# Kernel tuning notes

Measured on AMD Instinct MI355X. Metric: run time of the kernel, lower is better.

The kernel has to match this reference:

```python
import jax, jax.numpy as jnp
import numpy as np

N_NODES = 50000
N_EDGES = 400000
IN_CH = 5
HID = 64
HEADS = 8
NEG_SLOPE = 0.2  # PyG GATConv default


def _gat_layer(x, src, dst, n, W, a_src, a_dst, b, heads, C, concat):
    """PyG-style GATConv (eval mode, add_self_loops already applied to src/dst)."""
    h = (x @ W).reshape(n, heads, C)                      # [N,H,C]
    s_src = jnp.sum(h * a_src, axis=-1)                   # [N,H]
    s_dst = jnp.sum(h * a_dst, axis=-1)                   # [N,H]
    e = jax.nn.leaky_relu(s_src[src] + s_dst[dst], NEG_SLOPE)  # [E,H]
    # segment softmax over incoming edges of each dst node
    m = jax.ops.segment_max(e, dst, num_segments=n)       # [N,H]
    m = jnp.where(jnp.isfinite(m), m, 0.0)
    p = jnp.exp(e - m[dst])                               # [E,H]
    denom = jax.ops.segment_sum(p, dst, num_segments=n)   # [N,H]
    alpha = p / (denom[dst] + 1e-16)                      # [E,H]
    msg = alpha[:, :, None] * h[src]                      # [E,H,C]
    out = jax.ops.segment_sum(msg, dst, num_segments=n)   # [N,H,C]
    out = out.reshape(n, heads * C) if concat else out.mean(axis=1)
    return out + b


def setup_inputs() -> dict:
    key = jax.random.key(0)
    ks = jax.random.split(key, 16)
    g = lambda k, shape, fan: jax.random.normal(k, shape, jnp.float32) * (1.0 / np.sqrt(fan))
    x = jax.random.normal(ks[0], (N_NODES, IN_CH), jnp.float32)
    edge_index = jax.random.randint(ks[1], (2, N_EDGES), 0, N_NODES, dtype=jnp.int64)
    d = {
        "x": x,
        "edge_index": edge_index,
        # layer 1: in=5 -> 8 heads x 64
        "W1": g(ks[2], (IN_CH, HEADS * HID), IN_CH),
        "as1": g(ks[3], (HEADS, HID), HID),
        "ad1": g(ks[4], (HEADS, HID), HID),
        "b1": jnp.zeros((HEADS * HID,), jnp.float32),
        # layer 2: in=512 -> 8 heads x 64
        "W2": g(ks[5], (HEADS * HID, HEADS * HID), HEADS * HID),
        "as2": g(ks[6], (HEADS, HID), HID),
        "ad2": g(ks[7], (HEADS, HID), HID),
        "b2": jnp.zeros((HEADS * HID,), jnp.float32),
        # layer 3: in=512 -> 1 head x 64
        "W3": g(ks[8], (HEADS * HID, HID), HEADS * HID),
        "as3": g(ks[9], (1, HID), HID),
        "ad3": g(ks[10], (1, HID), HID),
        "b3": jnp.zeros((HID,), jnp.float32),
        # classifier
        "Wc": g(ks[11], (HID, 1), HID),
        "bc": jnp.zeros((1,), jnp.float32),
    }
    return d


def reference(x, edge_index, W1, as1, ad1, b1, W2, as2, ad2, b2, W3, as3, ad3, b3, Wc, bc):
    n = x.shape[0]
    loop = jnp.arange(n, dtype=edge_index.dtype)
    src = jnp.concatenate([edge_index[0], loop])  # PyG add_self_loops=True
    dst = jnp.concatenate([edge_index[1], loop])
    h = jax.nn.elu(_gat_layer(x, src, dst, n, W1, as1, ad1, b1, HEADS, HID, True))
    h = jax.nn.elu(_gat_layer(h, src, dst, n, W2, as2, ad2, b2, HEADS, HID, True))
    h = jax.nn.elu(_gat_layer(h, src, dst, n, W3, as3, ad3, b3, 1, HID, True))
    logits = h @ Wc + bc                               # [N,1]
    return jax.nn.sigmoid(logits).squeeze(-1)          # [N]
```

## Files before the change

kernel.cpp:

```cpp
#include <hip/hip_runtime.h>
#include <hip/hip_bf16.h>
#include <math.h>

#define N_NODES 50000
#define N_EDGES 400000
#define E_TOT   (N_EDGES + N_NODES)
#define HEADS   8
#define HID     64
#define HC      (HEADS * HID)
#define NBLK    ((N_NODES + 255) / 256)

typedef __attribute__((ext_vector_type(8))) short bf16x8;
typedef __attribute__((ext_vector_type(4))) float f32x4;

__device__ __forceinline__ float elu1(float x) { return x > 0.f ? x : __expf(x) - 1.f; }

__device__ __forceinline__ unsigned short f2bf(float x) {
    unsigned u = __float_as_uint(x);
    unsigned r = (u + 0x7FFFu + ((u >> 16) & 1u)) >> 16;
    return (unsigned short)r;
}
__device__ __forceinline__ float bf2f(unsigned short h) {
    return __uint_as_float(((unsigned)h) << 16);
}

__global__ void hist_kernel(const int* __restrict__ dst, int* __restrict__ deg) {
    int e = blockIdx.x * blockDim.x + threadIdx.x;
    if (e >= E_TOT) return;
    int d = (e < N_EDGES) ? dst[e] : (e - N_EDGES);
    atomicAdd(&deg[d], 1);
}

__global__ __launch_bounds__(256) void deg_partial_kernel(const int* __restrict__ deg,
                                                          int* __restrict__ psum) {
    __shared__ int sm[256];
    int t = threadIdx.x;
    int idx = blockIdx.x * 256 + t;
    int v = (idx < N_NODES) ? deg[idx] : 0;
    sm[t] = v;
    __syncthreads();
    for (int off = 128; off >= 1; off >>= 1) {
        if (t < off) sm[t] += sm[t + off];
        __syncthreads();
    }
    if (t == 0) psum[blockIdx.x] = sm[0];
}

__global__ __launch_bounds__(256) void scan_partial_kernel(int* __restrict__ psum) {
    __shared__ int sm[256];
    int t = threadIdx.x;
    int v = (t < NBLK) ? psum[t] : 0;
    sm[t] = v;
    __syncthreads();
    for (int off = 1; off < 256; off <<= 1) {
        int add = (t >= off) ? sm[t - off] : 0;
        __syncthreads();
        sm[t] += add;
        __syncthreads();
    }
    if (t < NBLK) psum[t] = sm[t] - v;
}

__global__ __launch_bounds__(256) void rowptr_kernel(const int* __restrict__ deg,
                                                     const int* __restrict__ psum,
                                                     int* __restrict__ rowptr,
                                                     int* __restrict__ cursor) {
    __shared__ int sm[256];
    int t = threadIdx.x;
    int idx = blockIdx.x * 256 + t;
    int v = (idx < N_NODES) ? deg[idx] : 0;
    sm[t] = v;
    __syncthreads();
    for (int off = 1; off < 256; off <<= 1) {
        int add = (t >= off) ? sm[t - off] : 0;
        __syncthreads();
        sm[t] += add;
        __syncthreads();
    }
    if (idx < N_NODES) {
        int r = psum[blockIdx.x] + sm[t] - v;
        rowptr[idx] = r;
        cursor[idx] = r;
    }
    if (idx == 0) rowptr[N_NODES] = E_TOT;
}

__global__ void scatter_kernel(const int* __restrict__ srcrow, const int* __restrict__ dstrow,
                               int* __restrict__ cursor, int* __restrict__ src_sorted) {
    int e = blockIdx.x * blockDim.x + threadIdx.x;
    if (e >= E_TOT) return;
    int s, d;
    if (e < N_EDGES) { s = srcrow[e]; d = dstrow[e]; }
    else             { s = d = e - N_EDGES; }
    int pos = atomicAdd(&cursor[d], 1);
    src_sorted[pos] = s;
}

__global__ __launch_bounds__(256) void gemm5score_kernel(
    const float* __restrict__ x, const float* __restrict__ W,
    const float* __restrict__ a_src, const float* __restrict__ a_dst,
    unsigned short* __restrict__ h, float* __restrict__ ssrc, float* __restrict__ sdst) {
    int wave = threadIdx.x >> 6, lane = threadIdx.x & 63;
    int n = blockIdx.x * 4 + wave;
    float xr[5];
#pragma unroll
    for (int k = 0; k < 5; ++k) xr[k] = x[n * 5 + k];
    int c0 = lane * 8;
    float hv[8];
#pragma unroll
    for (int q = 0; q < 8; ++q) {
        float acc = 0.f;
#pragma unroll
        for (int k = 0; k < 5; ++k) acc = fmaf(xr[k], W[k * 512 + c0 + q], acc);
        hv[q] = acc;
    }
    unsigned short hp[8];
#pragma unroll
    for (int q = 0; q < 8; ++q) hp[q] = f2bf(hv[q]);
    *(uint4*)(h + (size_t)n * 512 + c0) = *(const uint4*)hp;

    int head = lane >> 3;
    int cb = (lane & 7) * 8;
    float s1 = 0.f, s2 = 0.f;
#pragma unroll
    for (int q = 0; q < 8; ++q) {
        s1 = fmaf(hv[q], a_src[head * 64 + cb + q], s1);
        s2 = fmaf(hv[q], a_dst[head * 64 + cb + q], s2);
    }
#pragma unroll
    for (int step = 1; step <= 4; step <<= 1) {
        s1 += __shfl_xor(s1, step, 64);
        s2 += __shfl_xor(s2, step, 64);
    }
    if ((lane & 7) == 0) {
        ssrc[n * 8 + head] = s1;
        sdst[n * 8 + head] = s2;
    }
}

template <int NCOL>
__global__ void wtrans_kernel(const float* __restrict__ W, unsigned short* __restrict__ hi) {
    int idx = blockIdx.x * 256 + threadIdx.x;
    if (idx >= 512 * NCOL) return;
    int k = idx / NCOL, n = idx % NCOL;
    hi[(size_t)n * 512 + k] = f2bf(W[idx]);
}

template <int ROWS, int NW>
__device__ __forceinline__ void stage_pair(const unsigned short* __restrict__ src, int row0,
                                           int maxRow, int k0, char* lds0, char* lds1,
                                           int wave, int lane) {
    constexpr int CHUNKS = ROWS / 16;
    for (int c = wave; c < CHUNKS; c += NW) {
        int r = c * 16 + (lane >> 2);
        int p = lane & 3;
        int g = p ^ ((r >> 1) & 3);
        int gr = row0 + r;
        if (gr > maxRow) gr = maxRow;
        const unsigned short* gp = src + (size_t)gr * 512 + k0 + g * 8;
        __builtin_amdgcn_global_load_lds((const __attribute__((address_space(1))) void*)gp,
                                         (__attribute__((address_space(3))) void*)(lds0 + c * 1024),
                                         16, 0, 0);
        __builtin_amdgcn_global_load_lds((const __attribute__((address_space(1))) void*)(gp + 32),
                                         (__attribute__((address_space(3))) void*)(lds1 + c * 1024),
                                         16, 0, 0);
    }
}

template <int BM, int BN, int WM, int WN, int GX, int SH, bool SCORE>
__global__ __launch_bounds__(WM * WN * 64) void gemm_mfma(
    const unsigned short* __restrict__ A, const unsigned short* __restrict__ B,
    unsigned short* __restrict__ C,
    const float* __restrict__ asrc, const float* __restrict__ adst,
    float* __restrict__ ssrc, float* __restrict__ sdst,
    int M, int Nout, int maxRowB) {
    constexpr int NW = WM * WN;
    constexpr int MI = BM / (16 * WM);
    constexpr int NI = BN / (16 * WN);
    static_assert(!SCORE || NI * 16 == 64, "score epilogue needs 64 cols per wave");
    constexpr int ABYTES = BM * 64;
    constexpr int BBYTES = BN * 64;
    constexpr int GRPS = GX * 8;
    __shared__ __attribute__((aligned(16))) char lds[(ABYTES + BBYTES) * 2];
    char* const pA0 = lds;
    char* const pA1 = pA0 + ABYTES;
    char* const pB0 = pA1 + ABYTES;
    char* const pB1 = pB0 + BBYTES;

    const int wg = blockIdx.x;
    const int bx = (wg % GRPS) >> 3;
    const int by = (wg / GRPS) * 8 + (wg & 7);
    if (by * BM >= M) return;
    const int m0 = by * BM, n0 = bx * BN;

    const int t = threadIdx.x, lane = t & 63, wave = t >> 6;
    const int wr = wave / WN, wc = wave % WN;

    int offA[MI], offB[NI];
#pragma unroll
    for (int s = 0; s < MI; ++s) {
        int rA = (wr * MI + s) * 16 + (lane & 15);
        offA[s] = rA * 64 + ((((lane >> 4) ^ ((rA >> 1) & 3))) << 4);
    }
#pragma unroll
    for (int s = 0; s < NI; ++s) {
        int rB = (wc * NI + s) * 16 + (lane & 15);
        offB[s] = rB * 64 + ((((lane >> 4) ^ ((rB >> 1) & 3))) << 4);
    }

    f32x4 acc[MI][NI] = {};

    for (int k0 = 0; k0 < 512; k0 += 64) {
        stage_pair<BM, NW>(A, m0, M - 1,   k0, pA0, pA1, wave, lane);
        stage_pair<BN, NW>(B, n0, maxRowB, k0, pB0, pB1, wave, lane);
        __syncthreads();

#pragma unroll
        for (int half = 0; half < 2; ++half) {
            const char* cA = half ? pA1 : pA0;
            const char* cB = half ? pB1 : pB0;
            bf16x8 av[MI], bv[NI];
#pragma unroll
            for (int s = 0; s < MI; ++s) av[s] = *(const bf16x8*)(cA + offA[s]);
#pragma unroll
            for (int s = 0; s < NI; ++s) bv[s] = *(const bf16x8*)(cB + offB[s]);
#pragma unroll
            for (int i = 0; i < MI; ++i)
#pragma unroll
                for (int j = 0; j < NI; ++j)
                    acc[i][j] = __builtin_amdgcn_mfma_f32_16x16x32_bf16(av[i], bv[j], acc[i][j], 0, 0, 0);
        }
        __syncthreads();
    }

#pragma unroll
    for (int i = 0; i < MI; ++i) {
        int row = m0 + (wr * MI + i) * 16 + ((lane >> 4) << 2);
#pragma unroll
        for (int j = 0; j < NI; ++j) {
            int col = n0 + (wc * NI + j) * 16 + (lane & 15);
            f32x4 v = acc[i][j];
#pragma unroll
            for (int r = 0; r < 4; ++r) {
                if (row + r < M) C[(size_t)(row + r) * Nout + col] = f2bf(v[r]);
            }
        }
    }

    if constexpr (SCORE) {
        const int head = n0 / 64 + wc;
        float aS[NI], aD[NI];
#pragma unroll
        for (int j = 0; j < NI; ++j) {
            int cl = j * 16 + (lane & 15);
            aS[j] = asrc[head * 64 + cl];
            aD[j] = adst[head * 64 + cl];
        }
        float Ps[MI][4], Pd[MI][4];
#pragma unroll
        for (int i = 0; i < MI; ++i)
#pragma unroll
            for (int r = 0; r < 4; ++r) { Ps[i][r] = 0.f; Pd[i][r] = 0.f; }
#pragma unroll
        for (int i = 0; i < MI; ++i)
#pragma unroll
            for (int j = 0; j < NI; ++j)
#pragma unroll
                for (int r = 0; r < 4; ++r) {
                    Ps[i][r] = fmaf(acc[i][j][r], aS[j], Ps[i][r]);
                    Pd[i][r] = fmaf(acc[i][j][r], aD[j], Pd[i][r]);
                }
#pragma unroll
        for (int step = 1; step <= 8; step <<= 1) {
#pragma unroll
            for (int i = 0; i < MI; ++i)
#pragma unroll
                for (int r = 0; r < 4; ++r) {
                    Ps[i][r] += __shfl_xor(Ps[i][r], step, 64);
                    Pd[i][r] += __shfl_xor(Pd[i][r], step, 64);
                }
        }
        int idx = lane & 15, g = lane >> 4;
        if (idx < MI * 4) {
            float vs = 0.f, vd = 0.f;
#pragma unroll
            for (int i = 0; i < MI; ++i)
#pragma unroll
                for (int r = 0; r < 4; ++r) {
                    bool sel = (idx == i * 4 + r);
                    vs = sel ? Ps[i][r] : vs;
                    vd = sel ? Pd[i][r] : vd;
                }
            int ii = idx >> 2, rr = idx & 3;
            int row = m0 + (wr * MI + ii) * 16 + g * 4 + rr;
            if (row < M) {
                ssrc[(size_t)row * SH + head] = vs;
                sdst[(size_t)row * SH + head] = vd;
            }
        }
    }
}

template <int H>
__global__ void softmax_kernel(const int* __restrict__ rowptr, const int* __restrict__ srcs,
                               const float* __restrict__ ssrc, const float* __restrict__ sdst,
                               float* __restrict__ p, float* __restrict__ rden) {
    int gid = blockIdx.x * blockDim.x + threadIdx.x;
    if (gid >= N_NODES * H) return;
    int n = gid / H, hh = gid % H;
    int lo = rowptr[n], hi = rowptr[n + 1];
    float sd = sdst[gid];
    float su0 = 0.f, su1 = 0.f, su2 = 0.f, su3 = 0.f;
    int j = lo;
    for (; j + 4 <= hi; j += 4) {
        int s0 = srcs[j], s1 = srcs[j + 1], s2 = srcs[j + 2], s3 = srcs[j + 3];
        float v0 = ssrc[s0 * H + hh] + sd;
        float v1 = ssrc[s1 * H + hh] + sd;
        float v2 = ssrc[s2 * H + hh] + sd;
        float v3 = ssrc[s3 * H + hh] + sd;
        v0 = v0 > 0.f ? v0 : 0.2f * v0;
        v1 = v1 > 0.f ? v1 : 0.2f * v1;
        v2 = v2 > 0.f ? v2 : 0.2f * v2;
        v3 = v3 > 0.f ? v3 : 0.2f * v3;
        float e0 = __expf(v0), e1 = __expf(v1), e2 = __expf(v2), e3 = __expf(v3);
        p[(size_t)j * H + hh] = e0;
        p[(size_t)(j + 1) * H + hh] = e1;
        p[(size_t)(j + 2) * H + hh] = e2;
        p[(size_t)(j + 3) * H + hh] = e3;
        su0 += e0; su1 += e1; su2 += e2; su3 += e3;
    }
    for (; j < hi; ++j) {
        float v = ssrc[srcs[j] * H + hh] + sd;
        v = v > 0.f ? v : 0.2f * v;
        float e = __expf(v);
        p[(size_t)j * H + hh] = e;
        su0 += e;
    }
    float sum = (su0 + su1) + (su2 + su3);
    rden[gid] = 1.f / (sum + 1e-16f);
}

__global__ __launch_bounds__(256) void agg8_kernel(const unsigned short* __restrict__ h,
                                                   const float* __restrict__ p,
                                                   const int* __restrict__ rowptr,
                                                   const int* __restrict__ srcs,
                                                   const float* __restrict__ rden,
                                                   const float* __restrict__ bias,
                                                   unsigned short* __restrict__ out) {
    int n = blockIdx.x;
    int t = threadIdx.x;
    int hh = t >> 5;
    int lo = rowptr[n], hi = rowptr[n + 1];
    float rd = rden[n * 8 + hh];
    float a0 = 0.f, a1 = 0.f, b0 = 0.f, b1 = 0.f;
    float c0 = 0.f, c1 = 0.f, d0 = 0.f, d1 = 0.f;
    int j = lo;
    for (; j + 4 <= hi; j += 4) {
        int s0 = srcs[j], s1 = srcs[j + 1], s2 = srcs[j + 2], s3 = srcs[j + 3];
        unsigned v0 = *(const unsigned*)(h + (size_t)s0 * 512 + 2 * t);
        unsigned v1 = *(const unsigned*)(h + (size_t)s1 * 512 + 2 * t);
        unsigned v2 = *(const unsigned*)(h + (size_t)s2 * 512 + 2 * t);
        unsigned v3 = *(const unsigned*)(h + (size_t)s3 * 512 + 2 * t);
        float p0 = p[(size_t)j * 8 + hh];
        float p1 = p[(size_t)(j + 1) * 8 + hh];
        float p2 = p[(size_t)(j + 2) * 8 + hh];
        float p3 = p[(size_t)(j + 3) * 8 + hh];
        a0 = fmaf(p0, bf2f((unsigned short)(v0 & 0xffff)), a0);
        a1 = fmaf(p0, bf2f((unsigned short)(v0 >> 16)), a1);
        b0 = fmaf(p1, bf2f((unsigned short)(v1 & 0xffff)), b0);
        b1 = fmaf(p1, bf2f((unsigned short)(v1 >> 16)), b1);
        c0 = fmaf(p2, bf2f((unsigned short)(v2 & 0xffff)), c0);
        c1 = fmaf(p2, bf2f((unsigned short)(v2 >> 16)), c1);
        d0 = fmaf(p3, bf2f((unsigned short)(v3 & 0xffff)), d0);
        d1 = fmaf(p3, bf2f((unsigned short)(v3 >> 16)), d1);
    }
    for (; j < hi; ++j) {
        int s = srcs[j];
        unsigned v = *(const unsigned*)(h + (size_t)s * 512 + 2 * t);
        float pj = p[(size_t)j * 8 + hh];
        a0 = fmaf(pj, bf2f((unsigned short)(v & 0xffff)), a0);
        a1 = fmaf(pj, bf2f((unsigned short)(v >> 16)), a1);
    }
    float s0 = (a0 + b0) + (c0 + d0);
    float s1 = (a1 + b1) + (c1 + d1);
    float2 bv = *(const float2*)(bias + 2 * t);
    float v0 = elu1(s0 * rd + bv.x);
    float v1 = elu1(s1 * rd + bv.y);
    unsigned pack = (unsigned)f2bf(v0) | ((unsigned)f2bf(v1) << 16);
    *(unsigned*)(out + (size_t)n * 512 + 2 * t) = pack;
}

__global__ __launch_bounds__(64) void agg1cls_kernel(const unsigned short* __restrict__ h,
                                                     const float* __restrict__ p,
                                                     const int* __restrict__ rowptr,
                                                     const int* __restrict__ srcs,
                                                     const float* __restrict__ rden,
                                                     const float* __restrict__ bias,
                                                     const float* __restrict__ Wc,
                                                     const float* __restrict__ bc,
                                                     float* __restrict__ out) {
    int n = blockIdx.x;
    int t = threadIdx.x;
    int lo = rowptr[n], hi = rowptr[n + 1];
    float rd = rden[n];
    float a = 0.f, b = 0.f, c = 0.f, d = 0.f;
    int j = lo;
    for (; j + 4 <= hi; j += 4) {
        int s0 = srcs[j], s1 = srcs[j + 1], s2 = srcs[j + 2], s3 = srcs[j + 3];
        float h0 = bf2f(h[(size_t)s0 * 64 + t]);
        float h1 = bf2f(h[(size_t)s1 * 64 + t]);
        float h2 = bf2f(h[(size_t)s2 * 64 + t]);
        float h3 = bf2f(h[(size_t)s3 * 64 + t]);
        a = fmaf(p[j], h0, a);
        b = fmaf(p[j + 1], h1, b);
        c = fmaf(p[j + 2], h2, c);
        d = fmaf(p[j + 3], h3, d);
    }
    for (; j < hi; ++j) {
        a = fmaf(p[j], bf2f(h[(size_t)srcs[j] * 64 + t]), a);
    }
    float acc = (a + b) + (c + d);
    float v = elu1(acc * rd + bias[t]);
    float prod = v * Wc[t];
#pragma unroll
    for (int off = 32; off >= 1; off >>= 1) prod += __shfl_down(prod, off);
    if (t == 0) out[n] = 1.f / (1.f + __expf(-(prod + bc[0])));
}

extern "C" void kernel_launch(void* const* d_in, const int* in_sizes, int n_in,
                              void* d_out, int out_size, void* d_ws, size_t ws_size,
                              hipStream_t stream) {
    const float* x   = (const float*)d_in[0];
    const int*   ei  = (const int*)d_in[1];
    const int* src_row = ei;
    const int* dst_row = ei + N_EDGES;
    const float* W1  = (const float*)d_in[2];
    const float* as1 = (const float*)d_in[3];
    const float* ad1 = (const float*)d_in[4];
    const float* b1  = (const float*)d_in[5];
    const float* W2  = (const float*)d_in[6];
    const float* as2 = (const float*)d_in[7];
    const float* ad2 = (const float*)d_in[8];
    const float* b2  = (const float*)d_in[9];
    const float* W3  = (const float*)d_in[10];
    const float* as3 = (const float*)d_in[11];
    const float* ad3 = (const float*)d_in[12];
    const float* b3  = (const float*)d_in[13];
    const float* Wc  = (const float*)d_in[14];
    const float* bc  = (const float*)d_in[15];

    char* w = (char*)d_ws;
    auto alloc = [&](size_t bytes) -> void* {
        void* ptr = (void*)w;
        w += (bytes + 255) & ~(size_t)255;
        return ptr;
    };
    int*   deg    = (int*)alloc((size_t)N_NODES * 4);
    int*   rowptr = (int*)alloc((size_t)(N_NODES + 1) * 4);
    int*   cursor = (int*)alloc((size_t)N_NODES * 4);
    int*   srcs   = (int*)alloc((size_t)E_TOT * 4);
    int*   psum   = (int*)alloc((size_t)NBLK * 4);
    float* pbuf   = (float*)alloc((size_t)E_TOT * HEADS * 4);
    float* ssrc   = (float*)alloc((size_t)N_NODES * HEADS * 4);
    float* sdst   = (float*)alloc((size_t)N_NODES * HEADS * 4);
    float* rden   = (float*)alloc((size_t)N_NODES * HEADS * 4);
    unsigned short* hbf = (unsigned short*)alloc((size_t)N_NODES * HC * 2);
    unsigned short* gbf = (unsigned short*)alloc((size_t)N_NODES * HC * 2);
    unsigned short* w2t = (unsigned short*)alloc((size_t)512 * 512 * 2);
    unsigned short* w3t = (unsigned short*)alloc((size_t)64 * 512 * 2);

    hipMemsetAsync(deg, 0, (size_t)N_NODES * 4, stream);

    const int EB = (E_TOT + 255) / 256;
    hist_kernel<<<EB, 256, 0, stream>>>(dst_row, deg);
    deg_partial_kernel<<<NBLK, 256, 0, stream>>>(deg, psum);
    scan_partial_kernel<<<1, 256, 0, stream>>>(psum);
    rowptr_kernel<<<NBLK, 256, 0, stream>>>(deg, psum, rowptr, cursor);
    scatter_kernel<<<EB, 256, 0, stream>>>(src_row, dst_row, cursor, srcs);

    wtrans_kernel<512><<<(512 * 512 + 255) / 256, 256, 0, stream>>>(W2, w2t);
    wtrans_kernel<64><<<(512 * 64 + 255) / 256, 256, 0, stream>>>(W3, w3t);

    const int NHB = (N_NODES * HEADS + 255) / 256;
    const int NB  = (N_NODES + 255) / 256;
    const int MB128 = (N_NODES + 127) / 128;
    const int G2 = ((MB128 + 7) / 8) * 32;
    const int MB64 = (N_NODES + 63) / 64;
    const int G3 = ((MB64 + 7) / 8) * 8;

    gemm5score_kernel<<<N_NODES / 4, 256, 0, stream>>>(x, W1, as1, ad1, hbf, ssrc, sdst);
    softmax_kernel<8><<<NHB, 256, 0, stream>>>(rowptr, srcs, ssrc, sdst, pbuf, rden);
    agg8_kernel<<<N_NODES, 256, 0, stream>>>(hbf, pbuf, rowptr, srcs, rden, b1, gbf);

    gemm_mfma<128, 128, 2, 2, 4, 8, true><<<G2, 256, 0, stream>>>(
        gbf, w2t, hbf, as2, ad2, ssrc, sdst, N_NODES, 512, 511);
    softmax_kernel<8><<<NHB, 256, 0, stream>>>(rowptr, srcs, ssrc, sdst, pbuf, rden);
    agg8_kernel<<<N_NODES, 256, 0, stream>>>(hbf, pbuf, rowptr, srcs, rden, b2, gbf);

    gemm_mfma<64, 64, 2, 1, 1, 1, true><<<G3, 128, 0, stream>>>(
        gbf, w3t, hbf, as3, ad3, ssrc, sdst, N_NODES, 64, 63);
    softmax_kernel<1><<<NB, 256, 0, stream>>>(rowptr, srcs, ssrc, sdst, pbuf, rden);
    agg1cls_kernel<<<N_NODES, 64, 0, stream>>>(hbf, pbuf, rowptr, srcs, rden, b3, Wc, bc,
                                               (float*)d_out);
}
```

Before: 439.5 us.

## Fuse edge softmax into aggregation kernels, recomputing attention weights inline

Removes the separate softmax kernels and the per-edge probability buffer. Each aggregation block now recomputes leaky-relu and exp of the edge scores from ssrc/sdst while it gathers neighbor features, accumulating the denominator alongside and normalizing at the end. This saves a kernel launch per layer and the write and reread of a large E×H float buffer. In exchange, every one of the 32 threads per head redundantly evaluates exp for each edge. The existing code also skips the max subtraction, which this change keeps.

```diff
diff --git a/kernel.cpp b/kernel.cpp
--- a/kernel.cpp
+++ b/kernel.cpp
@@ -301,59 +301,21 @@
     }
 }
 
-template <int H>
-__global__ void softmax_kernel(const int* __restrict__ rowptr, const int* __restrict__ srcs,
-                               const float* __restrict__ ssrc, const float* __restrict__ sdst,
-                               float* __restrict__ p, float* __restrict__ rden) {
-    int gid = blockIdx.x * blockDim.x + threadIdx.x;
-    if (gid >= N_NODES * H) return;
-    int n = gid / H, hh = gid % H;
-    int lo = rowptr[n], hi = rowptr[n + 1];
-    float sd = sdst[gid];
-    float su0 = 0.f, su1 = 0.f, su2 = 0.f, su3 = 0.f;
-    int j = lo;
-    for (; j + 4 <= hi; j += 4) {
-        int s0 = srcs[j], s1 = srcs[j + 1], s2 = srcs[j + 2], s3 = srcs[j + 3];
-        float v0 = ssrc[s0 * H + hh] + sd;
-        float v1 = ssrc[s1 * H + hh] + sd;
-        float v2 = ssrc[s2 * H + hh] + sd;
-        float v3 = ssrc[s3 * H + hh] + sd;
-        v0 = v0 > 0.f ? v0 : 0.2f * v0;
-        v1 = v1 > 0.f ? v1 : 0.2f * v1;
-        v2 = v2 > 0.f ? v2 : 0.2f * v2;
-        v3 = v3 > 0.f ? v3 : 0.2f * v3;
-        float e0 = __expf(v0), e1 = __expf(v1), e2 = __expf(v2), e3 = __expf(v3);
-        p[(size_t)j * H + hh] = e0;
-        p[(size_t)(j + 1) * H + hh] = e1;
-        p[(size_t)(j + 2) * H + hh] = e2;
-        p[(size_t)(j + 3) * H + hh] = e3;
-        su0 += e0; su1 += e1; su2 += e2; su3 += e3;
-    }
-    for (; j < hi; ++j) {
-        float v = ssrc[srcs[j] * H + hh] + sd;
-        v = v > 0.f ? v : 0.2f * v;
-        float e = __expf(v);
-        p[(size_t)j * H + hh] = e;
-        su0 += e;
-    }
-    float sum = (su0 + su1) + (su2 + su3);
-    rden[gid] = 1.f / (sum + 1e-16f);
-}
-
-__global__ __launch_bounds__(256) void agg8_kernel(const unsigned short* __restrict__ h,
-                                                   const float* __restrict__ p,
-                                                   const int* __restrict__ rowptr,
-                                                   const int* __restrict__ srcs,
-                                                   const float* __restrict__ rden,
-                                                   const float* __restrict__ bias,
-                                                   unsigned short* __restrict__ out) {
+__global__ __launch_bounds__(256) void agg8sf_kernel(const unsigned short* __restrict__ h,
+                                                     const float* __restrict__ ssrc,
+                                                     const float* __restrict__ sdst,
+                                                     const int* __restrict__ rowptr,
+                                                     const int* __restrict__ srcs,
+                                                     const float* __restrict__ bias,
+                                                     unsigned short* __restrict__ out) {
     int n = blockIdx.x;
     int t = threadIdx.x;
     int hh = t >> 5;
     int lo = rowptr[n], hi = rowptr[n + 1];
-    float rd = rden[n * 8 + hh];
+    float sd = sdst[n * 8 + hh];
     float a0 = 0.f, a1 = 0.f, b0 = 0.f, b1 = 0.f;
     float c0 = 0.f, c1 = 0.f, d0 = 0.f, d1 = 0.f;
+    float q0 = 0.f, q1 = 0.f, q2 = 0.f, q3 = 0.f;
     int j = lo;
     for (; j + 4 <= hi; j += 4) {
         int s0 = srcs[j], s1 = srcs[j + 1], s2 = srcs[j + 2], s3 = srcs[j + 3];
@@ -361,10 +323,16 @@
         unsigned v1 = *(const unsigned*)(h + (size_t)s1 * 512 + 2 * t);
         unsigned v2 = *(const unsigned*)(h + (size_t)s2 * 512 + 2 * t);
         unsigned v3 = *(const unsigned*)(h + (size_t)s3 * 512 + 2 * t);
-        float p0 = p[(size_t)j * 8 + hh];
-        float p1 = p[(size_t)(j + 1) * 8 + hh];
-        float p2 = p[(size_t)(j + 2) * 8 + hh];
-        float p3 = p[(size_t)(j + 3) * 8 + hh];
+        float e0 = ssrc[s0 * 8 + hh] + sd;
+        float e1 = ssrc[s1 * 8 + hh] + sd;
+        float e2 = ssrc[s2 * 8 + hh] + sd;
+        float e3 = ssrc[s3 * 8 + hh] + sd;
+        e0 = e0 > 0.f ? e0 : 0.2f * e0;
+        e1 = e1 > 0.f ? e1 : 0.2f * e1;
+        e2 = e2 > 0.f ? e2 : 0.2f * e2;
+        e3 = e3 > 0.f ? e3 : 0.2f * e3;
+        float p0 = __expf(e0), p1 = __expf(e1), p2 = __expf(e2), p3 = __expf(e3);
+        q0 += p0; q1 += p1; q2 += p2; q3 += p3;
         a0 = fmaf(p0, bf2f((unsigned short)(v0 & 0xffff)), a0);
         a1 = fmaf(p0, bf2f((unsigned short)(v0 >> 16)), a1);
         b0 = fmaf(p1, bf2f((unsigned short)(v1 & 0xffff)), b0);
@@ -377,10 +345,15 @@
     for (; j < hi; ++j) {
         int s = srcs[j];
         unsigned v = *(const unsigned*)(h + (size_t)s * 512 + 2 * t);
-        float pj = p[(size_t)j * 8 + hh];
-        a0 = fmaf(pj, bf2f((unsigned short)(v & 0xffff)), a0);
-        a1 = fmaf(pj, bf2f((unsigned short)(v >> 16)), a1);
-    }
+        float e = ssrc[s * 8 + hh] + sd;
+        e = e > 0.f ? e : 0.2f * e;
+        float p = __expf(e);
+        q0 += p;
+        a0 = fmaf(p, bf2f((unsigned short)(v & 0xffff)), a0);
+        a1 = fmaf(p, bf2f((unsigned short)(v >> 16)), a1);
+    }
+    float sum = (q0 + q1) + (q2 + q3);
+    float rd = 1.f / (sum + 1e-16f);
     float s0 = (a0 + b0) + (c0 + d0);
     float s1 = (a1 + b1) + (c1 + d1);
     float2 bv = *(const float2*)(bias + 2 * t);
@@ -391,10 +364,10 @@
 }
 
 __global__ __launch_bounds__(64) void agg1cls_kernel(const unsigned short* __restrict__ h,
-                                                     const float* __restrict__ p,
+                                                     const float* __restrict__ ssrc,
+                                                     const float* __restrict__ sdst,
                                                      const int* __restrict__ rowptr,
                                                      const int* __restrict__ srcs,
-                                                     const float* __restrict__ rden,
                                                      const float* __restrict__ bias,
                                                      const float* __restrict__ Wc,
                                                      const float* __restrict__ bc,
@@ -402,8 +375,9 @@
     int n = blockIdx.x;
     int t = threadIdx.x;
     int lo = rowptr[n], hi = rowptr[n + 1];
-    float rd = rden[n];
+    float sd = sdst[n];
     float a = 0.f, b = 0.f, c = 0.f, d = 0.f;
+    float q0 = 0.f, q1 = 0.f, q2 = 0.f, q3 = 0.f;
     int j = lo;
     for (; j + 4 <= hi; j += 4) {
         int s0 = srcs[j], s1 = srcs[j + 1], s2 = srcs[j + 2], s3 = srcs[j + 3];
@@ -411,14 +385,28 @@
         float h1 = bf2f(h[(size_t)s1 * 64 + t]);
         float h2 = bf2f(h[(size_t)s2 * 64 + t]);
         float h3 = bf2f(h[(size_t)s3 * 64 + t]);
-        a = fmaf(p[j], h0, a);
-        b = fmaf(p[j + 1], h1, b);
-        c = fmaf(p[j + 2], h2, c);
-        d = fmaf(p[j + 3], h3, d);
+        float e0 = ssrc[s0] + sd, e1 = ssrc[s1] + sd, e2 = ssrc[s2] + sd, e3 = ssrc[s3] + sd;
+        e0 = e0 > 0.f ? e0 : 0.2f * e0;
+        e1 = e1 > 0.f ? e1 : 0.2f * e1;
+        e2 = e2 > 0.f ? e2 : 0.2f * e2;
+        e3 = e3 > 0.f ? e3 : 0.2f * e3;
+        float p0 = __expf(e0), p1 = __expf(e1), p2 = __expf(e2), p3 = __expf(e3);
+        q0 += p0; q1 += p1; q2 += p2; q3 += p3;
+        a = fmaf(p0, h0, a);
+        b = fmaf(p1, h1, b);
+        c = fmaf(p2, h2, c);
+        d = fmaf(p3, h3, d);
     }
     for (; j < hi; ++j) {
-        a = fmaf(p[j], bf2f(h[(size_t)srcs[j] * 64 + t]), a);
-    }
+        int s = srcs[j];
+        float e = ssrc[s] + sd;
+        e = e > 0.f ? e : 0.2f * e;
+        float p = __expf(e);
+        q0 += p;
+        a = fmaf(p, bf2f(h[(size_t)s * 64 + t]), a);
+    }
+    float sum = (q0 + q1) + (q2 + q3);
+    float rd = 1.f / (sum + 1e-16f);
     float acc = (a + b) + (c + d);
     float v = elu1(acc * rd + bias[t]);
     float prod = v * Wc[t];
@@ -460,10 +448,8 @@
     int*   cursor = (int*)alloc((size_t)N_NODES * 4);
     int*   srcs   = (int*)alloc((size_t)E_TOT * 4);
     int*   psum   = (int*)alloc((size_t)NBLK * 4);
-    float* pbuf   = (float*)alloc((size_t)E_TOT * HEADS * 4);
     float* ssrc   = (float*)alloc((size_t)N_NODES * HEADS * 4);
     float* sdst   = (float*)alloc((size_t)N_NODES * HEADS * 4);
-    float* rden   = (float*)alloc((size_t)N_NODES * HEADS * 4);
     unsigned short* hbf = (unsigned short*)alloc((size_t)N_NODES * HC * 2);
     unsigned short* gbf = (unsigned short*)alloc((size_t)N_NODES * HC * 2);
     unsigned short* w2t = (unsigned short*)alloc((size_t)512 * 512 * 2);
@@ -481,7 +467,6 @@
     wtrans_kernel<512><<<(512 * 512 + 255) / 256, 256, 0, stream>>>(W2, w2t);
     wtrans_kernel<64><<<(512 * 64 + 255) / 256, 256, 0, stream>>>(W3, w3t);
 
-    const int NHB = (N_NODES * HEADS + 255) / 256;
     const int NB  = (N_NODES + 255) / 256;
     const int MB128 = (N_NODES + 127) / 128;
     const int G2 = ((MB128 + 7) / 8) * 32;
@@ -489,17 +474,14 @@
     const int G3 = ((MB64 + 7) / 8) * 8;
 
     gemm5score_kernel<<<N_NODES / 4, 256, 0, stream>>>(x, W1, as1, ad1, hbf, ssrc, sdst);
-    softmax_kernel<8><<<NHB, 256, 0, stream>>>(rowptr, srcs, ssrc, sdst, pbuf, rden);
-    agg8_kernel<<<N_NODES, 256, 0, stream>>>(hbf, pbuf, rowptr, srcs, rden, b1, gbf);
+    agg8sf_kernel<<<N_NODES, 256, 0, stream>>>(hbf, ssrc, sdst, rowptr, srcs, b1, gbf);
 
     gemm_mfma<128, 128, 2, 2, 4, 8, true><<<G2, 256, 0, stream>>>(
         gbf, w2t, hbf, as2, ad2, ssrc, sdst, N_NODES, 512, 511);
-    softmax_kernel<8><<<NHB, 256, 0, stream>>>(rowptr, srcs, ssrc, sdst, pbuf, rden);
-    agg8_kernel<<<N_NODES, 256, 0, stream>>>(hbf, pbuf, rowptr, srcs, rden, b2, gbf);
+    agg8sf_kernel<<<N_NODES, 256, 0, stream>>>(hbf, ssrc, sdst, rowptr, srcs, b2, gbf);
 
     gemm_mfma<64, 64, 2, 1, 1, 1, true><<<G3, 128, 0, stream>>>(
         gbf, w3t, hbf, as3, ad3, ssrc, sdst, N_NODES, 64, 63);
-    softmax_kernel<1><<<NB, 256, 0, stream>>>(rowptr, srcs, ssrc, sdst, pbuf, rden);
-    agg1cls_kernel<<<N_NODES, 64, 0, stream>>>(hbf, pbuf, rowptr, srcs, rden, b3, Wc, bc,
+    agg1cls_kernel<<<N_NODES, 64, 0, stream>>>(hbf, ssrc, sdst, rowptr, srcs, b3, Wc, bc,
                                                (float*)d_out);
 }
```

Result: faster. 424.4 us (-3.4%).
